# Optimization experiments

Measured on AMD Instinct MI355X. Metric: run time of the kernel, lower is better.

The kernel has to match this reference:

```python
import jax, jax.numpy as jnp
import numpy as np
from jax import lax

D_CONV = 4


def setup_inputs() -> dict:
    key = jax.random.key(0)
    ks = jax.random.split(key, 8)
    b, L, d_model = 2, 1024, 1024
    d_inner, d_state = 2048, 16
    s = 0.02  # weight scale
    return {
        "x": jax.random.normal(ks[0], (b, L, d_model), jnp.float32),
        "in_w": jax.random.normal(ks[1], (2 * d_inner, d_model), jnp.float32) * s,
        "in_b": jnp.zeros((2 * d_inner,), jnp.float32),
        "conv_w": jax.random.normal(ks[2], (d_inner, 1, D_CONV), jnp.float32) * s,
        "conv_b": jnp.zeros((d_inner,), jnp.float32),
        "xproj_w": jax.random.normal(ks[3], (2 * d_state + 1, d_inner), jnp.float32) * s,
        "dt_w": jax.random.normal(ks[4], (d_inner, 1), jnp.float32) * s,
        "dt_b": jnp.zeros((d_inner,), jnp.float32),
        "A_log": jax.random.normal(ks[5], (d_inner, d_state), jnp.float32),
        "D": jnp.ones((d_inner,), jnp.float32),
        "out_w": jax.random.normal(ks[6], (d_model, d_inner), jnp.float32) * s,
    }


def reference(x, in_w, in_b, conv_w, conv_b, xproj_w, dt_w, dt_b, A_log, D, out_w):
    b, L, _ = x.shape
    d_inner = conv_w.shape[0]
    d_state = A_log.shape[1]

    xz = x @ in_w.T + in_b                       # (b, L, 2*d_inner)
    xh, z = jnp.split(xz, 2, axis=-1)            # each (b, L, d_inner)

    # depthwise causal conv1d (torch pads d_conv-1 both sides then slices [:L])
    xc = jnp.transpose(xh, (0, 2, 1))            # (b, d_inner, L)
    xc = lax.conv_general_dilated(
        xc, conv_w, window_strides=(1,), padding=[(D_CONV - 1, 0)],
        feature_group_count=d_inner, dimension_numbers=("NCH", "OIH", "NCH"))
    xc = xc + conv_b[None, :, None]
    xh = jnp.transpose(xc, (0, 2, 1))            # (b, L, d_inner)

    xh = xh * jax.nn.silu(z)

    proj = xh @ xproj_w.T                        # (b, L, 2*d_state+1)
    dlt = proj[..., :1]                          # (b, L, 1)
    B = proj[..., 1:1 + d_state]                 # (b, L, d_state)
    C = proj[..., 1 + d_state:]                  # (b, L, d_state)

    # dt_proj: (b,L,1) -> (b,L,d_inner); source applies softplus then exp
    delta = jnp.exp(jax.nn.softplus(dlt @ dt_w.T + dt_b))  # (b, L, d_inner)

    A = -jnp.exp(A_log)                          # (d_inner, d_state)

    def step(h, inp):
        xt, dt, Bt, Ct = inp                     # (b,i), (b,i), (b,s), (b,s)
        A_bar = jnp.exp(A[None] * dt[..., None])          # (b, i, s)
        B_bar = dt[..., None] * Bt[:, None, :]            # (b, i, s)
        h = A_bar * h + B_bar * xt[..., None]             # (b, i, s)
        yt = jnp.einsum("bis,bs->bi", h, Ct)              # (b, i)
        return h, yt

    h0 = jnp.zeros((b, d_inner, d_state), x.dtype)
    xs = (jnp.moveaxis(xh, 1, 0), jnp.moveaxis(delta, 1, 0),
          jnp.moveaxis(B, 1, 0), jnp.moveaxis(C, 1, 0))
    _, ys = lax.scan(step, h0, xs)               # (L, b, d_inner)
    y = jnp.moveaxis(ys, 0, 1) + D * xh          # (b, L, d_inner)

    return y @ out_w.T                           # (b, L, d_model)
```

## Files before the change

### kernel.cpp

```cpp
#include <hip/hip_runtime.h>
#include <hip/hip_bf16.h>

#define NTOK   2048
#define DMODEL 1024
#define DINNER 2048
#define DSTATE 16
#define SEQLEN 1024
#define NPROJ  33
#define CCH    32
#define CT     32

typedef __attribute__((ext_vector_type(8))) short bf16x8;
typedef __attribute__((ext_vector_type(4))) float f32x4;
typedef __attribute__((ext_vector_type(8))) unsigned short us8;

__device__ __forceinline__ unsigned short f2bf(float f) {
  unsigned u = __float_as_uint(f);
  return (unsigned short)((u + 0x7FFFu + ((u >> 16) & 1u)) >> 16);
}

__device__ __forceinline__ void gload_lds16(const void* g, void* l) {
  __builtin_amdgcn_global_load_lds(
      (const __attribute__((address_space(1))) unsigned int*)g,
      (__attribute__((address_space(3))) unsigned int*)l, 16, 0, 0);
}

__global__ __launch_bounds__(256) void cast3_bf16_kernel(
    const float* __restrict__ s0, const float* __restrict__ s1,
    const float* __restrict__ s2, unsigned short* __restrict__ dst) {
  const int idx = (blockIdx.x * 256 + threadIdx.x) * 8;
  const float* src;
  int off;
  if (idx < (NTOK * DMODEL)) { src = s0; off = idx; }
  else if (idx < (NTOK * DMODEL + 2 * DINNER * DMODEL)) {
    src = s1; off = idx - NTOK * DMODEL;
  } else { src = s2; off = idx - (NTOK * DMODEL + 2 * DINNER * DMODEL); }
  const float4 a = *(const float4*)(src + off);
  const float4 b = *(const float4*)(src + off + 4);
  us8 o;
  o[0] = f2bf(a.x); o[1] = f2bf(a.y); o[2] = f2bf(a.z); o[3] = f2bf(a.w);
  o[4] = f2bf(b.x); o[5] = f2bf(b.y); o[6] = f2bf(b.z); o[7] = f2bf(b.w);
  *(us8*)(dst + idx) = o;
}

template <int BN>
__global__ __launch_bounds__(256) void gemm_bt_mfma(
    const unsigned short* __restrict__ A, const unsigned short* __restrict__ B,
    const float* __restrict__ bias, float* __restrict__ C, int M, int K) {
  constexpr int TN = BN / 32;
  __shared__ unsigned short As[2][128 * 32];
  __shared__ unsigned short Bs[2][BN * 32];

  const int tid = threadIdx.x;
  const int wid = tid >> 6;
  const int lane = tid & 63;
  const int n0 = blockIdx.x * 128;
  const int m0 = blockIdx.y * BN;

  const int wave_m = wid & 1;
  const int wave_n = wid >> 1;
  const int lm = lane & 15;
  const int lq = lane >> 4;

  f32x4 acc[4][TN] = {};

  for (int k0 = 0; k0 < K; k0 += 64) {
    __syncthreads();
#pragma unroll
    for (int h = 0; h < 2; ++h) {
      const int kh = k0 + h * 32;
#pragma unroll
      for (int j = 0; j < 2; ++j) {
        const int cb = j * 256 + wid * 64;
        const int c = cb + lane;
        gload_lds16(A + (size_t)(n0 + (c >> 2)) * K + kh + (c & 3) * 8,
                    &As[h][cb * 8]);
      }
#pragma unroll
      for (int j = 0; j < BN / 64; ++j) {
        const int cb = j * 256 + wid * 64;
        const int c = cb + lane;
        gload_lds16(B + (size_t)(m0 + (c >> 2)) * K + kh + (c & 3) * 8,
                    &Bs[h][cb * 8]);
      }
    }
    __syncthreads();

#pragma unroll
    for (int h = 0; h < 2; ++h) {
      bf16x8 af[4], bfr[TN];
#pragma unroll
      for (int tm = 0; tm < 4; ++tm)
        af[tm] = *(const bf16x8*)
            &As[h][(wave_m * 64 + tm * 16 + lm) * 32 + lq * 8];
#pragma unroll
      for (int tn = 0; tn < TN; ++tn)
        bfr[tn] = *(const bf16x8*)
            &Bs[h][(wave_n * (BN / 2) + tn * 16 + lm) * 32 + lq * 8];
#pragma unroll
      for (int tm = 0; tm < 4; ++tm)
#pragma unroll
        for (int tn = 0; tn < TN; ++tn)
          acc[tm][tn] = __builtin_amdgcn_mfma_f32_16x16x32_bf16(
              af[tm], bfr[tn], acc[tm][tn], 0, 0, 0);
    }
  }

#pragma unroll
  for (int tm = 0; tm < 4; ++tm) {
    const int row = n0 + wave_m * 64 + tm * 16 + lq * 4;
#pragma unroll
    for (int tn = 0; tn < TN; ++tn) {
      const int col = m0 + wave_n * (BN / 2) + tn * 16 + lm;
      const float bv = bias ? bias[col] : 0.f;
#pragma unroll
      for (int r = 0; r < 4; ++r)
        C[(size_t)(row + r) * M + col] = acc[tm][tn][r] + bv;
    }
  }
}

__global__ __launch_bounds__(256) void conv_xproj_kernel(
    const float* __restrict__ xz, const float* __restrict__ cw,
    const float* __restrict__ cb, const float* __restrict__ w,
    float* __restrict__ xg, float* __restrict__ proj) {
  __shared__ float red[NPROJ][4][4];
  const int tid = threadIdx.x;
  const int wid = tid >> 6;
  const int lane = tid & 63;
  const int n0 = blockIdx.x * 4;
  const int l0 = n0 & (SEQLEN - 1);

  float xgv[4][8];
#pragma unroll
  for (int j = 0; j < 8; ++j) {
    const int i = tid + 256 * j;
    const float4 w4 = ((const float4*)cw)[i];
    const float cbv = cb[i];
    float taps[7];
#pragma unroll
    for (int d = 0; d < 7; ++d) {
      const bool valid = (l0 != 0) || (d >= 3);
      taps[d] = valid ? xz[(size_t)(n0 - 3 + d) * (2 * DINNER) + i] : 0.f;
    }
#pragma unroll
    for (int tok = 0; tok < 4; ++tok) {
      float acc = cbv;
      acc = fmaf(w4.x, taps[tok + 0], acc);
      acc = fmaf(w4.y, taps[tok + 1], acc);
      acc = fmaf(w4.z, taps[tok + 2], acc);
      acc = fmaf(w4.w, taps[tok + 3], acc);
      const float z = xz[(size_t)(n0 + tok) * (2 * DINNER) + DINNER + i];
      const float sig = 1.f / (1.f + __expf(-z));
      const float v = acc * (z * sig);
      xgv[tok][j] = v;
      xg[(size_t)(n0 + tok) * DINNER + i] = v;
    }
  }

  for (int r = 0; r < NPROJ; ++r) {
    float p0 = 0.f, p1 = 0.f, p2 = 0.f, p3 = 0.f;
#pragma unroll
    for (int j = 0; j < 8; ++j) {
      const float wv = w[(size_t)r * DINNER + tid + 256 * j];
      p0 = fmaf(xgv[0][j], wv, p0);
      p1 = fmaf(xgv[1][j], wv, p1);
      p2 = fmaf(xgv[2][j], wv, p2);
      p3 = fmaf(xgv[3][j], wv, p3);
    }
#pragma unroll
    for (int off = 32; off >= 1; off >>= 1) {
      p0 += __shfl_down(p0, off, 64);
      p1 += __shfl_down(p1, off, 64);
      p2 += __shfl_down(p2, off, 64);
      p3 += __shfl_down(p3, off, 64);
    }
    if (lane == 0) {
      red[r][0][wid] = p0; red[r][1][wid] = p1;
      red[r][2][wid] = p2; red[r][3][wid] = p3;
    }
  }
  __syncthreads();
  if (tid < NPROJ * 4) {
    const int r = tid >> 2;
    const int tok = tid & 3;
    const float s = red[r][tok][0] + red[r][tok][1] +
                    red[r][tok][2] + red[r][tok][3];
    proj[(size_t)(n0 + tok) * NPROJ + r] = s;
  }
}

__global__ __launch_bounds__(256) void scan_phase1(
    const float* __restrict__ xg, const float* __restrict__ proj,
    const float* __restrict__ dt_w, const float* __restrict__ dt_b,
    const float* __restrict__ A_log,
    float* __restrict__ Sbuf, float* __restrict__ Hbuf) {
  __shared__ float pl[CT][36];
  const int tid = threadIdx.x;
  const int i = blockIdx.x * 256 + tid;
  const int k = blockIdx.y;
  const int b = blockIdx.z;
  const int n0 = b * SEQLEN + k * CT;

  for (int e = tid; e < CT * NPROJ; e += 256) {
    const int t = e / NPROJ;
    const int c = e - t * NPROJ;
    pl[t][c] = proj[(size_t)(n0 + t) * NPROJ + c];
  }
  __syncthreads();

  const float dtw = dt_w[i], dtb = dt_b[i];
  float Av[DSTATE];
#pragma unroll
  for (int s = 0; s < DSTATE; ++s) Av[s] = -__expf(A_log[i * DSTATE + s]);

  float h[DSTATE] = {};
  float Ssum = 0.f;

  for (int t = 0; t < CT; ++t) {
    float fr[20];
#pragma unroll
    for (int j = 0; j < 5; ++j) {
      const float4 v = *(const float4*)&pl[t][j * 4];
      fr[4 * j + 0] = v.x; fr[4 * j + 1] = v.y;
      fr[4 * j + 2] = v.z; fr[4 * j + 3] = v.w;
    }
    const float delta = 1.f + __expf(fmaf(fr[0], dtw, dtb));
    Ssum += delta;
    const float x = xg[(size_t)(n0 + t) * DINNER + i];
    const float dx = delta * x;
#pragma unroll
    for (int s = 0; s < DSTATE; ++s)
      h[s] = fmaf(__expf(Av[s] * delta), h[s], fr[1 + s] * dx);
  }

  const size_t ck = (size_t)(b * CCH + k) * DINNER + i;
  Sbuf[ck] = Ssum;
  float4* Hq = (float4*)(Hbuf + ck * DSTATE);
#pragma unroll
  for (int q = 0; q < 4; ++q)
    Hq[q] = make_float4(h[4 * q], h[4 * q + 1], h[4 * q + 2], h[4 * q + 3]);
}

__global__ __launch_bounds__(256) void scan_phase2(
    const float* __restrict__ A_log, const float* __restrict__ Sbuf,
    float* __restrict__ Hbuf) {
  const int gid = blockIdx.x * 256 + threadIdx.x;
  const int s = gid & (DSTATE - 1);
  const int i = (gid >> 4) & (DINNER - 1);
  const int b = gid >> 15;
  const float Av = -__expf(A_log[i * DSTATE + s]);
  float H = 0.f;
  for (int k = 0; k < CCH; ++k) {
    const size_t ck = (size_t)(b * CCH + k) * DINNER + i;
    const float hk = Hbuf[ck * DSTATE + s];
    const float a = __expf(Av * Sbuf[ck]);
    Hbuf[ck * DSTATE + s] = H;
    H = fmaf(a, H, hk);
  }
}

__global__ __launch_bounds__(256) void scan_phase3(
    const float* __restrict__ xg, const float* __restrict__ proj,
    const float* __restrict__ dt_w, const float* __restrict__ dt_b,
    const float* __restrict__ A_log, const float* __restrict__ Dp,
    const float* __restrict__ Hbuf, unsigned short* __restrict__ y) {
  __shared__ float pl[CT][36];
  const int tid = threadIdx.x;
  const int i = blockIdx.x * 256 + tid;
  const int k = blockIdx.y;
  const int b = blockIdx.z;
  const int n0 = b * SEQLEN + k * CT;

  for (int e = tid; e < CT * NPROJ; e += 256) {
    const int t = e / NPROJ;
    const int c = e - t * NPROJ;
    pl[t][c] = proj[(size_t)(n0 + t) * NPROJ + c];
  }
  __syncthreads();

  const float dtw = dt_w[i], dtb = dt_b[i];
  const float Dv = Dp[i];
  float Av[DSTATE];
#pragma unroll
  for (int s = 0; s < DSTATE; ++s) Av[s] = -__expf(A_log[i * DSTATE + s]);

  const size_t ck = (size_t)(b * CCH + k) * DINNER + i;
  float h[DSTATE];
  const float4* Hq = (const float4*)(Hbuf + ck * DSTATE);
#pragma unroll
  for (int q = 0; q < 4; ++q) {
    const float4 v = Hq[q];
    h[4 * q + 0] = v.x; h[4 * q + 1] = v.y;
    h[4 * q + 2] = v.z; h[4 * q + 3] = v.w;
  }

  for (int t = 0; t < CT; ++t) {
    float fr[33];
#pragma unroll
    for (int j = 0; j < 8; ++j) {
      const float4 v = *(const float4*)&pl[t][j * 4];
      fr[4 * j + 0] = v.x; fr[4 * j + 1] = v.y;
      fr[4 * j + 2] = v.z; fr[4 * j + 3] = v.w;
    }
    fr[32] = pl[t][32];
    const float delta = 1.f + __expf(fmaf(fr[0], dtw, dtb));
    const float x = xg[(size_t)(n0 + t) * DINNER + i];
    const float dx = delta * x;
    float yt = 0.f;
#pragma unroll
    for (int s = 0; s < DSTATE; ++s) {
      h[s] = fmaf(__expf(Av[s] * delta), h[s], fr[1 + s] * dx);
      yt = fmaf(h[s], fr[17 + s], yt);
    }
    y[(size_t)(n0 + t) * DINNER + i] = f2bf(fmaf(Dv, x, yt));
  }
}

extern "C" void kernel_launch(void* const* d_in, const int* in_sizes, int n_in,
                              void* d_out, int out_size, void* d_ws, size_t ws_size,
                              hipStream_t stream) {
  const float* x       = (const float*)d_in[0];
  const float* in_w    = (const float*)d_in[1];
  const float* in_b    = (const float*)d_in[2];
  const float* conv_w  = (const float*)d_in[3];
  const float* conv_b  = (const float*)d_in[4];
  const float* xproj_w = (const float*)d_in[5];
  const float* dt_w    = (const float*)d_in[6];
  const float* dt_b    = (const float*)d_in[7];
  const float* A_log   = (const float*)d_in[8];
  const float* Dp      = (const float*)d_in[9];
  const float* out_w   = (const float*)d_in[10];
  float* out = (float*)d_out;

  float* ws = (float*)d_ws;
  float* xz   = ws;
  float* xg   = ws + 8388608;
  unsigned short* bf_base = (unsigned short*)(ws + 12582912);
  unsigned short* x_bf    = bf_base;
  unsigned short* inw_bf  = bf_base + (size_t)NTOK * DMODEL;
  unsigned short* outw_bf = bf_base + (size_t)NTOK * DMODEL + 2 * DINNER * DMODEL;
  unsigned short* yb_bf   = (unsigned short*)(ws + 16777216);
  float* proj = ws + 18874368;
  float* Sbuf = ws + 19398656;
  float* Hbuf = ws + 19922944;

  cast3_bf16_kernel<<<(8 * 1024 * 1024) / (256 * 8), 256, 0, stream>>>(
      x, in_w, out_w, bf_base);

  gemm_bt_mfma<128><<<dim3(NTOK / 128, (2 * DINNER) / 128), 256, 0, stream>>>(
      x_bf, inw_bf, in_b, xz, 2 * DINNER, DMODEL);

  conv_xproj_kernel<<<NTOK / 4, 256, 0, stream>>>(
      xz, conv_w, conv_b, xproj_w, xg, proj);

  scan_phase1<<<dim3(DINNER / 256, CCH, 2), 256, 0, stream>>>(
      xg, proj, dt_w, dt_b, A_log, Sbuf, Hbuf);
  scan_phase2<<<(2 * DINNER * DSTATE) / 256, 256, 0, stream>>>(
      A_log, Sbuf, Hbuf);
  scan_phase3<<<dim3(DINNER / 256, CCH, 2), 256, 0, stream>>>(
      xg, proj, dt_w, dt_b, A_log, Dp, Hbuf, yb_bf);

  gemm_bt_mfma<64><<<dim3(NTOK / 128, DMODEL / 64), 256, 0, stream>>>(
      yb_bf, outw_bf, nullptr, out, DMODEL, DINNER);
}
```

Measured before the change: 239.2 us.

## Split conv/gate from x-projection and run x-projection as split-K bf16 MFMA GEMM

Splits the fused conv+xproj kernel into a wider-grid conv/gate kernel, which also writes a bf16 copy of the gated activations, and a split-K MFMA GEMM against a zero-padded bf16 xproj weight. A small reduction kernel then sums the partial results. The scan chunking also changes from 32 chunks of 32 tokens to 64 chunks of 16. The aim is to replace the scalar FMA and shuffle reduction with matrix cores and to raise parallelism. The cost is two extra launches, extra workspace traffic, and reduced precision on the projection inputs.

```diff
diff --git a/kernel.cpp b/kernel.cpp
--- a/kernel.cpp
+++ b/kernel.cpp
@@ -7,8 +7,10 @@
 #define DSTATE 16
 #define SEQLEN 1024
 #define NPROJ  33
-#define CCH    32
-#define CT     32
+#define NPAD   48
+#define KSPLIT 16
+#define CCH    64
+#define CT     16
 
 typedef __attribute__((ext_vector_type(8))) short bf16x8;
 typedef __attribute__((ext_vector_type(4))) float f32x4;
@@ -25,16 +27,29 @@
       (__attribute__((address_space(3))) unsigned int*)l, 16, 0, 0);
 }
 
-__global__ __launch_bounds__(256) void cast3_bf16_kernel(
+#define CAST_N0 (NTOK * DMODEL)
+#define CAST_N1 (CAST_N0 + 2 * DINNER * DMODEL)
+#define CAST_N2 (CAST_N1 + DMODEL * DINNER)
+#define CAST_N3 (CAST_N2 + NPAD * DINNER)
+__global__ __launch_bounds__(256) void cast4_bf16_kernel(
     const float* __restrict__ s0, const float* __restrict__ s1,
-    const float* __restrict__ s2, unsigned short* __restrict__ dst) {
+    const float* __restrict__ s2, const float* __restrict__ s3,
+    unsigned short* __restrict__ dst) {
   const int idx = (blockIdx.x * 256 + threadIdx.x) * 8;
   const float* src;
   int off;
-  if (idx < (NTOK * DMODEL)) { src = s0; off = idx; }
-  else if (idx < (NTOK * DMODEL + 2 * DINNER * DMODEL)) {
-    src = s1; off = idx - NTOK * DMODEL;
-  } else { src = s2; off = idx - (NTOK * DMODEL + 2 * DINNER * DMODEL); }
+  if (idx < CAST_N0) { src = s0; off = idx; }
+  else if (idx < CAST_N1) { src = s1; off = idx - CAST_N0; }
+  else if (idx < CAST_N2) { src = s2; off = idx - CAST_N1; }
+  else {
+    off = idx - CAST_N2;
+    if (off >= NPROJ * DINNER) {
+      us8 z = {0, 0, 0, 0, 0, 0, 0, 0};
+      *(us8*)(dst + idx) = z;
+      return;
+    }
+    src = s3;
+  }
   const float4 a = *(const float4*)(src + off);
   const float4 b = *(const float4*)(src + off + 4);
   us8 o;
@@ -120,74 +135,113 @@
   }
 }
 
-__global__ __launch_bounds__(256) void conv_xproj_kernel(
+__global__ __launch_bounds__(256) void conv_gate_kernel(
     const float* __restrict__ xz, const float* __restrict__ cw,
-    const float* __restrict__ cb, const float* __restrict__ w,
-    float* __restrict__ xg, float* __restrict__ proj) {
-  __shared__ float red[NPROJ][4][4];
+    const float* __restrict__ cb, float* __restrict__ xg,
+    unsigned short* __restrict__ xgb) {
+  const int i = blockIdx.y * 256 + threadIdx.x;
+  const int n0 = blockIdx.x * 4;
+  const int l0 = n0 & (SEQLEN - 1);
+
+  const float4 w4 = ((const float4*)cw)[i];
+  const float cbv = cb[i];
+  float taps[7];
+#pragma unroll
+  for (int d = 0; d < 7; ++d) {
+    const bool valid = (l0 != 0) || (d >= 3);
+    taps[d] = valid ? xz[(size_t)(n0 - 3 + d) * (2 * DINNER) + i] : 0.f;
+  }
+#pragma unroll
+  for (int tok = 0; tok < 4; ++tok) {
+    float acc = cbv;
+    acc = fmaf(w4.x, taps[tok + 0], acc);
+    acc = fmaf(w4.y, taps[tok + 1], acc);
+    acc = fmaf(w4.z, taps[tok + 2], acc);
+    acc = fmaf(w4.w, taps[tok + 3], acc);
+    const float z = xz[(size_t)(n0 + tok) * (2 * DINNER) + DINNER + i];
+    const float sig = 1.f / (1.f + __expf(-z));
+    const float v = acc * (z * sig);
+    const size_t o = (size_t)(n0 + tok) * DINNER + i;
+    xg[o] = v;
+    xgb[o] = f2bf(v);
+  }
+}
+
+__global__ __launch_bounds__(256) void xproj_mfma_kernel(
+    const unsigned short* __restrict__ xgb, const unsigned short* __restrict__ wp,
+    float* __restrict__ pp) {
+  __shared__ unsigned short As[128 * 32];
+  __shared__ unsigned short Bs[NPAD * 32];
+
   const int tid = threadIdx.x;
   const int wid = tid >> 6;
   const int lane = tid & 63;
-  const int n0 = blockIdx.x * 4;
-  const int l0 = n0 & (SEQLEN - 1);
-
-  float xgv[4][8];
-#pragma unroll
-  for (int j = 0; j < 8; ++j) {
-    const int i = tid + 256 * j;
-    const float4 w4 = ((const float4*)cw)[i];
-    const float cbv = cb[i];
-    float taps[7];
-#pragma unroll
-    for (int d = 0; d < 7; ++d) {
-      const bool valid = (l0 != 0) || (d >= 3);
-      taps[d] = valid ? xz[(size_t)(n0 - 3 + d) * (2 * DINNER) + i] : 0.f;
-    }
-#pragma unroll
-    for (int tok = 0; tok < 4; ++tok) {
-      float acc = cbv;
-      acc = fmaf(w4.x, taps[tok + 0], acc);
-      acc = fmaf(w4.y, taps[tok + 1], acc);
-      acc = fmaf(w4.z, taps[tok + 2], acc);
-      acc = fmaf(w4.w, taps[tok + 3], acc);
-      const float z = xz[(size_t)(n0 + tok) * (2 * DINNER) + DINNER + i];
-      const float sig = 1.f / (1.f + __expf(-z));
-      const float v = acc * (z * sig);
-      xgv[tok][j] = v;
-      xg[(size_t)(n0 + tok) * DINNER + i] = v;
-    }
-  }
-
-  for (int r = 0; r < NPROJ; ++r) {
-    float p0 = 0.f, p1 = 0.f, p2 = 0.f, p3 = 0.f;
-#pragma unroll
-    for (int j = 0; j < 8; ++j) {
-      const float wv = w[(size_t)r * DINNER + tid + 256 * j];
-      p0 = fmaf(xgv[0][j], wv, p0);
-      p1 = fmaf(xgv[1][j], wv, p1);
-      p2 = fmaf(xgv[2][j], wv, p2);
-      p3 = fmaf(xgv[3][j], wv, p3);
-    }
-#pragma unroll
-    for (int off = 32; off >= 1; off >>= 1) {
-      p0 += __shfl_down(p0, off, 64);
-      p1 += __shfl_down(p1, off, 64);
-      p2 += __shfl_down(p2, off, 64);
-      p3 += __shfl_down(p3, off, 64);
-    }
-    if (lane == 0) {
-      red[r][0][wid] = p0; red[r][1][wid] = p1;
-      red[r][2][wid] = p2; red[r][3][wid] = p3;
-    }
-  }
-  __syncthreads();
-  if (tid < NPROJ * 4) {
-    const int r = tid >> 2;
-    const int tok = tid & 3;
-    const float s = red[r][tok][0] + red[r][tok][1] +
-                    red[r][tok][2] + red[r][tok][3];
-    proj[(size_t)(n0 + tok) * NPROJ + r] = s;
-  }
+  const int n0 = blockIdx.x * 128;
+  const int kbase = blockIdx.y * (DINNER / KSPLIT);
+
+  const int lm = lane & 15;
+  const int lq = lane >> 4;
+
+  f32x4 acc[2][3] = {};
+
+  for (int it = 0; it < (DINNER / KSPLIT) / 32; ++it) {
+    const int k0 = kbase + it * 32;
+    __syncthreads();
+#pragma unroll
+    for (int j = 0; j < 2; ++j) {
+      const int cb = j * 256 + wid * 64;
+      const int c = cb + lane;
+      gload_lds16(xgb + (size_t)(n0 + (c >> 2)) * DINNER + k0 + (c & 3) * 8,
+                  &As[cb * 8]);
+    }
+    if (wid < 3) {
+      const int cb = wid * 64;
+      const int c = cb + lane;
+      gload_lds16(wp + (size_t)(c >> 2) * DINNER + k0 + (c & 3) * 8,
+                  &Bs[cb * 8]);
+    }
+    __syncthreads();
+
+    bf16x8 af[2], bfr[3];
+#pragma unroll
+    for (int tm = 0; tm < 2; ++tm)
+      af[tm] = *(const bf16x8*)&As[(wid * 32 + tm * 16 + lm) * 32 + lq * 8];
+#pragma unroll
+    for (int tn = 0; tn < 3; ++tn)
+      bfr[tn] = *(const bf16x8*)&Bs[(tn * 16 + lm) * 32 + lq * 8];
+#pragma unroll
+    for (int tm = 0; tm < 2; ++tm)
+#pragma unroll
+      for (int tn = 0; tn < 3; ++tn)
+        acc[tm][tn] = __builtin_amdgcn_mfma_f32_16x16x32_bf16(
+            af[tm], bfr[tn], acc[tm][tn], 0, 0, 0);
+  }
+
+  float* base = pp + (size_t)blockIdx.y * NTOK * NPAD;
+#pragma unroll
+  for (int tm = 0; tm < 2; ++tm) {
+    const int row = n0 + wid * 32 + tm * 16 + lq * 4;
+#pragma unroll
+    for (int tn = 0; tn < 3; ++tn) {
+      const int col = tn * 16 + lm;
+#pragma unroll
+      for (int r = 0; r < 4; ++r)
+        base[(size_t)(row + r) * NPAD + col] = acc[tm][tn][r];
+    }
+  }
+}
+
+__global__ __launch_bounds__(256) void proj_reduce_kernel(
+    const float* __restrict__ pp, float* __restrict__ proj) {
+  const int gid = blockIdx.x * 256 + threadIdx.x;
+  if (gid >= NTOK * NPROJ) return;
+  const int n = gid / NPROJ;
+  const int r = gid - n * NPROJ;
+  float s = 0.f;
+#pragma unroll
+  for (int q = 0; q < KSPLIT; ++q)
+    s += pp[((size_t)q * NTOK + n) * NPAD + r];
+  proj[gid] = s;
 }
 
 __global__ __launch_bounds__(256) void scan_phase1(
@@ -334,25 +388,32 @@
   float* out = (float*)d_out;
 
   float* ws = (float*)d_ws;
-  float* xz   = ws;
-  float* xg   = ws + 8388608;
-  unsigned short* bf_base = (unsigned short*)(ws + 12582912);
+  float* xz = ws;
+  float* xg = ws + 8388608;
+  unsigned short* xgb = (unsigned short*)(ws + 12582912);
+  unsigned short* bf_base = (unsigned short*)(ws + 14680064);
   unsigned short* x_bf    = bf_base;
-  unsigned short* inw_bf  = bf_base + (size_t)NTOK * DMODEL;
-  unsigned short* outw_bf = bf_base + (size_t)NTOK * DMODEL + 2 * DINNER * DMODEL;
-  unsigned short* yb_bf   = (unsigned short*)(ws + 16777216);
-  float* proj = ws + 18874368;
-  float* Sbuf = ws + 19398656;
-  float* Hbuf = ws + 19922944;
-
-  cast3_bf16_kernel<<<(8 * 1024 * 1024) / (256 * 8), 256, 0, stream>>>(
-      x, in_w, out_w, bf_base);
+  unsigned short* inw_bf  = bf_base + CAST_N0;
+  unsigned short* outw_bf = bf_base + CAST_N1;
+  unsigned short* wpad_bf = bf_base + CAST_N2;
+  unsigned short* yb_bf = (unsigned short*)(ws + 19398656);
+  float* pp   = ws + 20971520;
+  float* proj = ws + 22544384;
+  float* Sbuf = ws + 23068672;
+  float* Hbuf = ws + 23592960;
+
+  cast4_bf16_kernel<<<CAST_N3 / (256 * 8), 256, 0, stream>>>(
+      x, in_w, out_w, xproj_w, bf_base);
 
   gemm_bt_mfma<128><<<dim3(NTOK / 128, (2 * DINNER) / 128), 256, 0, stream>>>(
       x_bf, inw_bf, in_b, xz, 2 * DINNER, DMODEL);
 
-  conv_xproj_kernel<<<NTOK / 4, 256, 0, stream>>>(
-      xz, conv_w, conv_b, xproj_w, xg, proj);
+  conv_gate_kernel<<<dim3(NTOK / 4, DINNER / 256), 256, 0, stream>>>(
+      xz, conv_w, conv_b, xg, xgb);
+
+  xproj_mfma_kernel<<<dim3(NTOK / 128, KSPLIT), 256, 0, stream>>>(
+      xgb, wpad_bf, pp);
+  proj_reduce_kernel<<<(NTOK * NPROJ + 255) / 256, 256, 0, stream>>>(pp, proj);
 
   scan_phase1<<<dim3(DINNER / 256, CCH, 2), 256, 0, stream>>>(
       xg, proj, dt_w, dt_b, A_log, Sbuf, Hbuf);
```

Result: faster. 222.7 us (-6.9%).
